# Performance work log

Hardware: AMD Instinct MI355X
Metric: run time of the kernel (lower is better)

Reference implementation:

```python
import jax, jax.numpy as jnp
import numpy as np

B, S, P, D = 32, 512, 512, 768

def setup_inputs() -> dict:
    key = jax.random.key(0)
    k1, k2 = jax.random.split(key)
    inputs = jax.random.normal(k1, (B, S, D), dtype=jnp.float32)
    prototypes = jax.random.normal(k2, (P, D), dtype=jnp.float32)
    return {"inputs": inputs, "prototypes": prototypes}

def reference(inputs, prototypes):
    # Squared Euclidean distance from every token vector to every prototype:
    # but the cross term is a GEMM and the huge [B,S,P,D] intermediate is never built).
    x_sq = jnp.sum(inputs * inputs, axis=-1, keepdims=True)          # [B, S, 1]
    p_sq = jnp.sum(prototypes * prototypes, axis=-1)                 # [P]
    cross = jnp.einsum('bsd,pd->bsp', inputs, prototypes)            # [B, S, P]
    distances = x_sq + p_sq[None, None, :] - 2.0 * cross             # [B, S, P]
    return (distances, prototypes)
```

## Files before the change

### kernel.cpp

```cpp
#include <hip/hip_runtime.h>
#include <hip/hip_bf16.h>


#define M_TOK 16384
#define N_PROT 512
#define K_DIM 768
#define BKC 128
#define NKC (K_DIM / BKC)
#define NSK (K_DIM / 32)
#define ASTR 136

typedef __attribute__((ext_vector_type(4))) float f32x4;
typedef __attribute__((ext_vector_type(8))) short bf16x8;

__device__ inline unsigned short f2bf(float f) {
    unsigned int u = __float_as_uint(f);
    u += 0x7fffu + ((u >> 16) & 1u);
    return (unsigned short)(u >> 16);
}

__global__ __launch_bounds__(256) void prep_b(
    const float* __restrict__ p,
    unsigned short* __restrict__ b_bf, float* __restrict__ p_sq,
    float* __restrict__ proto_out)
{
    const int row  = blockIdx.x * 4 + (threadIdx.x >> 6);
    const int lane = threadIdx.x & 63;

    const float4* src4 = (const float4*)(p + (size_t)row * K_DIM);
    unsigned short* dst = b_bf + (size_t)row * K_DIM;
    float4* pout4 = (float4*)(proto_out + (size_t)row * K_DIM);

    float ssum = 0.0f;
#pragma unroll
    for (int j = 0; j < 3; ++j) {
        const int idx = lane + j * 64;
        float4 v = src4[idx];
        ssum += v.x * v.x + v.y * v.y + v.z * v.z + v.w * v.w;
        ushort4 b;
        b.x = f2bf(v.x); b.y = f2bf(v.y); b.z = f2bf(v.z); b.w = f2bf(v.w);
        ((ushort4*)dst)[idx] = b;
        pout4[idx] = v;
    }
#pragma unroll
    for (int off = 32; off > 0; off >>= 1) ssum += __shfl_down(ssum, off);
    if (lane == 0) p_sq[row] = ssum;
}

__global__ __launch_bounds__(512, 4) void dist_main(
    const float* __restrict__ X,
    const unsigned short* __restrict__ Bb,
    const float* __restrict__ p_sq,
    float* __restrict__ out)
{
    __shared__ unsigned short lds_a[2][64 * ASTR];
    __shared__ float lds_xsq[64];

    const int bid     = blockIdx.x;
    const int logical = (bid & 7) * 64 + (bid >> 3);
    const int ms = logical >> 1;
    const int nh = logical & 1;
    const int bm = ms << 6;
    const int bn = nh << 8;

    const int tid  = threadIdx.x;
    const int wave = tid >> 6;
    const int lane = tid & 63;
    const int wn   = bn + (wave << 5);
    const int quad = lane >> 4;
    const int l16  = lane & 15;

    const int ar = tid >> 3;
    const int ac = tid & 7;
    const float* aptr = X + (size_t)(bm + ar) * K_DIM + ac * 4;

    float asq = 0.0f;

    {
        float4 v0 = *(const float4*)(aptr);
        float4 v1 = *(const float4*)(aptr + 32);
        float4 v2 = *(const float4*)(aptr + 64);
        float4 v3 = *(const float4*)(aptr + 96);
        float4 vv[4] = {v0, v1, v2, v3};
#pragma unroll
        for (int j = 0; j < 4; ++j) {
            float4 v = vv[j];
            asq += v.x * v.x + v.y * v.y + v.z * v.z + v.w * v.w;
            ushort4 u;
            u.x = f2bf(v.x); u.y = f2bf(v.y); u.z = f2bf(v.z); u.w = f2bf(v.w);
            *(ushort4*)&lds_a[0][ar * ASTR + (ac + 8 * j) * 4] = u;
        }
    }
    __syncthreads();

    const unsigned short* bp = Bb + (size_t)(wn + l16) * K_DIM + quad * 8;

    bf16x8 bcur0 = *(const bf16x8*)(bp);
    bf16x8 bcur1 = *(const bf16x8*)(bp + 16 * K_DIM);
    bf16x8 bnxt0, bnxt1;

    const f32x4 zero = {0.0f, 0.0f, 0.0f, 0.0f};
    f32x4 acc[4][2];
#pragma unroll
    for (int mt = 0; mt < 4; ++mt) {
        acc[mt][0] = zero; acc[mt][1] = zero;
    }

    for (int kc = 0; kc < NKC; ++kc) {
        float4 s0, s1, s2, s3;
        if (kc + 1 < NKC) {
            const float* ap = aptr + (kc + 1) * BKC;
            s0 = *(const float4*)(ap);
            s1 = *(const float4*)(ap + 32);
            s2 = *(const float4*)(ap + 64);
            s3 = *(const float4*)(ap + 96);
        }

#pragma unroll
        for (int s = 0; s < 4; ++s) {
            const int kk = kc * 4 + s;
            if (kk + 1 < NSK) {
                const int kn = (kk + 1) * 32;
                bnxt0 = *(const bf16x8*)(bp + kn);
                bnxt1 = *(const bf16x8*)(bp + 16 * K_DIM + kn);
            }

            bf16x8 af[4];
#pragma unroll
            for (int mt = 0; mt < 4; ++mt)
                af[mt] = *(const bf16x8*)&lds_a[kc & 1]
                    [(mt * 16 + l16) * ASTR + s * 32 + quad * 8];

#pragma unroll
            for (int mt = 0; mt < 4; ++mt) {
                acc[mt][0] = __builtin_amdgcn_mfma_f32_16x16x32_bf16(
                    af[mt], bcur0, acc[mt][0], 0, 0, 0);
                acc[mt][1] = __builtin_amdgcn_mfma_f32_16x16x32_bf16(
                    af[mt], bcur1, acc[mt][1], 0, 0, 0);
            }
            bcur0 = bnxt0; bcur1 = bnxt1;
        }

        if (kc + 1 < NKC) {
            unsigned short* aw = &lds_a[(kc + 1) & 1][ar * ASTR + ac * 4];
            float4 vv[4] = {s0, s1, s2, s3};
#pragma unroll
            for (int j = 0; j < 4; ++j) {
                float4 v = vv[j];
                asq += v.x * v.x + v.y * v.y + v.z * v.z + v.w * v.w;
                ushort4 u;
                u.x = f2bf(v.x); u.y = f2bf(v.y); u.z = f2bf(v.z); u.w = f2bf(v.w);
                *(ushort4*)(aw + 8 * j * 4) = u;
            }
        }
        __syncthreads();
    }

#pragma unroll
    for (int off = 1; off < 8; off <<= 1) asq += __shfl_xor(asq, off);
    if (ac == 0) lds_xsq[ar] = asq;
    __syncthreads();

    float ps0 = p_sq[wn + l16];
    float ps1 = p_sq[wn + 16 + l16];

#pragma unroll
    for (int mt = 0; mt < 4; ++mt) {
#pragma unroll
        for (int i = 0; i < 4; ++i) {
            const int lr = mt * 16 + quad * 4 + i;
            const float xs = lds_xsq[lr];
            float* orow = out + (size_t)(bm + lr) * N_PROT + wn + l16;
            orow[0]  = xs + ps0 - 2.0f * acc[mt][0][i];
            orow[16] = xs + ps1 - 2.0f * acc[mt][1][i];
        }
    }
}

extern "C" void kernel_launch(void* const* d_in, const int* in_sizes, int n_in,
                              void* d_out, int out_size, void* d_ws, size_t ws_size,
                              hipStream_t stream) {
    const float* inputs = (const float*)d_in[0];
    const float* protos = (const float*)d_in[1];
    float* out = (float*)d_out;
    float* proto_out = out + (size_t)M_TOK * N_PROT;

    char* ws = (char*)d_ws;
    unsigned short* b_bf = (unsigned short*)ws;
    float* p_sq = (float*)(ws + 786432);

    prep_b<<<128, 256, 0, stream>>>(protos, b_bf, p_sq, proto_out);
    dist_main<<<2 * (M_TOK / 64), 512, 0, stream>>>(inputs, b_bf, p_sq, out);
}
```

Baseline: 121.7 us.

## Swap MFMA operands for vectorized float4 stores and deepen B prefetch

The MFMA operands are swapped so prototypes act as the A operand and tokens as B. Each lane then holds four consecutive prototype columns for one token row, so the epilogue can write float4 stores instead of scalar ones. The global prefetch of the bf16 prototype fragments is also deepened from one to two k-steps ahead. The aim is to cut store instruction count, improve write coalescing and hide more global load latency, at the cost of extra VGPRs for the third buffer.

```diff
diff --git a/kernel.cpp b/kernel.cpp
--- a/kernel.cpp
+++ b/kernel.cpp
@@ -93,18 +93,20 @@
     }
     __syncthreads();
 
-    const unsigned short* bp = Bb + (size_t)(wn + l16) * K_DIM + quad * 8;
-
-    bf16x8 bcur0 = *(const bf16x8*)(bp);
-    bf16x8 bcur1 = *(const bf16x8*)(bp + 16 * K_DIM);
-    bf16x8 bnxt0, bnxt1;
+    const unsigned short* pb = Bb + (size_t)(wn + l16) * K_DIM + quad * 8;
+
+    bf16x8 A0[2], A1[2], A2[2];
+    A0[0] = *(const bf16x8*)(pb);
+    A0[1] = *(const bf16x8*)(pb + 16 * K_DIM);
+    A1[0] = *(const bf16x8*)(pb + 32);
+    A1[1] = *(const bf16x8*)(pb + 16 * K_DIM + 32);
 
     const f32x4 zero = {0.0f, 0.0f, 0.0f, 0.0f};
-    f32x4 acc[4][2];
-#pragma unroll
-    for (int mt = 0; mt < 4; ++mt) {
-        acc[mt][0] = zero; acc[mt][1] = zero;
-    }
+    f32x4 acc[2][4];
+#pragma unroll
+    for (int pt = 0; pt < 2; ++pt)
+#pragma unroll
+        for (int tt = 0; tt < 4; ++tt) acc[pt][tt] = zero;
 
     for (int kc = 0; kc < NKC; ++kc) {
         float4 s0, s1, s2, s3;
@@ -119,26 +121,27 @@
 #pragma unroll
         for (int s = 0; s < 4; ++s) {
             const int kk = kc * 4 + s;
-            if (kk + 1 < NSK) {
-                const int kn = (kk + 1) * 32;
-                bnxt0 = *(const bf16x8*)(bp + kn);
-                bnxt1 = *(const bf16x8*)(bp + 16 * K_DIM + kn);
+            if (kk + 2 < NSK) {
+                const int kn = (kk + 2) * 32;
+                A2[0] = *(const bf16x8*)(pb + kn);
+                A2[1] = *(const bf16x8*)(pb + 16 * K_DIM + kn);
             }
 
-            bf16x8 af[4];
-#pragma unroll
-            for (int mt = 0; mt < 4; ++mt)
-                af[mt] = *(const bf16x8*)&lds_a[kc & 1]
-                    [(mt * 16 + l16) * ASTR + s * 32 + quad * 8];
-
-#pragma unroll
-            for (int mt = 0; mt < 4; ++mt) {
-                acc[mt][0] = __builtin_amdgcn_mfma_f32_16x16x32_bf16(
-                    af[mt], bcur0, acc[mt][0], 0, 0, 0);
-                acc[mt][1] = __builtin_amdgcn_mfma_f32_16x16x32_bf16(
-                    af[mt], bcur1, acc[mt][1], 0, 0, 0);
+            bf16x8 tf[4];
+#pragma unroll
+            for (int tt = 0; tt < 4; ++tt)
+                tf[tt] = *(const bf16x8*)&lds_a[kc & 1]
+                    [(tt * 16 + l16) * ASTR + s * 32 + quad * 8];
+
+#pragma unroll
+            for (int tt = 0; tt < 4; ++tt) {
+                acc[0][tt] = __builtin_amdgcn_mfma_f32_16x16x32_bf16(
+                    A0[0], tf[tt], acc[0][tt], 0, 0, 0);
+                acc[1][tt] = __builtin_amdgcn_mfma_f32_16x16x32_bf16(
+                    A0[1], tf[tt], acc[1][tt], 0, 0, 0);
             }
-            bcur0 = bnxt0; bcur1 = bnxt1;
+            A0[0] = A1[0]; A0[1] = A1[1];
+            A1[0] = A2[0]; A1[1] = A2[1];
         }
 
         if (kc + 1 < NKC) {
@@ -161,19 +164,25 @@
     if (ac == 0) lds_xsq[ar] = asq;
     __syncthreads();
 
-    float ps0 = p_sq[wn + l16];
-    float ps1 = p_sq[wn + 16 + l16];
-
-#pragma unroll
-    for (int mt = 0; mt < 4; ++mt) {
-#pragma unroll
-        for (int i = 0; i < 4; ++i) {
-            const int lr = mt * 16 + quad * 4 + i;
-            const float xs = lds_xsq[lr];
-            float* orow = out + (size_t)(bm + lr) * N_PROT + wn + l16;
-            orow[0]  = xs + ps0 - 2.0f * acc[mt][0][i];
-            orow[16] = xs + ps1 - 2.0f * acc[mt][1][i];
-        }
+    float4 ps4[2];
+    ps4[0] = *(const float4*)&p_sq[wn + quad * 4];
+    ps4[1] = *(const float4*)&p_sq[wn + 16 + quad * 4];
+
+#pragma unroll
+    for (int tt = 0; tt < 4; ++tt) {
+        const float xs = lds_xsq[tt * 16 + l16];
+        float* orow = out + (size_t)(bm + tt * 16 + l16) * N_PROT + wn + quad * 4;
+        float4 o0, o1;
+        o0.x = xs + ps4[0].x - 2.0f * acc[0][tt][0];
+        o0.y = xs + ps4[0].y - 2.0f * acc[0][tt][1];
+        o0.z = xs + ps4[0].z - 2.0f * acc[0][tt][2];
+        o0.w = xs + ps4[0].w - 2.0f * acc[0][tt][3];
+        o1.x = xs + ps4[1].x - 2.0f * acc[1][tt][0];
+        o1.y = xs + ps4[1].y - 2.0f * acc[1][tt][1];
+        o1.z = xs + ps4[1].z - 2.0f * acc[1][tt][2];
+        o1.w = xs + ps4[1].w - 2.0f * acc[1][tt][3];
+        *(float4*)(orow)      = o0;
+        *(float4*)(orow + 16) = o1;
     }
 }
 
```

Measured after the change: 124.7 us. 1.02x slower.
